# Kernel optimization log

Measured on AMD Instinct MI355X. Metric: run time of the kernel, lower is better.

Reference implementation:

```python
import jax, jax.numpy as jnp
import numpy as np

EPS = 1e-7       # torchvision generalized_box_iou_loss eps
IMG_SIZE = 320.0  # labels are divided by 320 in the original criterion
NO_OBJ = 80       # class id 80 == no-object sentinel


def _hungarian(cost):
    """Jonker-Volgenant style shortest-augmenting-path LSA (== scipy.optimize.linear_sum_assignment).
    cost: [n, m] numpy array, n <= m. Returns (row_ind, col_ind) sorted by row."""
    cost = np.asarray(cost, dtype=np.float64)
    n, m = cost.shape
    INF = float("inf")
    u = np.zeros(n + 1)
    v = np.zeros(m + 1)
    p = np.zeros(m + 1, dtype=np.int64)   # p[j]: 1-based row matched to column j, 0 = free
    way = np.zeros(m + 1, dtype=np.int64)
    for i in range(1, n + 1):
        p[0] = i
        j0 = 0
        minv = np.full(m + 1, INF)
        used = np.zeros(m + 1, dtype=bool)
        while True:
            used[j0] = True
            i0 = p[j0]
            free = ~used[1:]
            cur = cost[i0 - 1] - u[i0] - v[1:]
            better = free & (cur < minv[1:])
            minv[1:] = np.where(better, cur, minv[1:])
            way[1:] = np.where(better, j0, way[1:])
            masked = np.where(free, minv[1:], INF)
            j1 = int(np.argmin(masked)) + 1
            delta = masked[j1 - 1]
            uj = np.nonzero(used)[0]
            u[p[uj]] += delta
            v[uj] -= delta
            minv[1:] = np.where(free, minv[1:] - delta, minv[1:])
            j0 = j1
            if p[j0] == 0:
                break
        while j0 != 0:
            j1 = way[j0]
            p[j0] = p[j1]
            j0 = j1
    cols = np.nonzero(p[1:])[0]
    rows = p[1:][cols] - 1
    order = np.argsort(rows)
    return rows[order], cols[order]


def _box_cxcywh_to_xyxy(b):
    cx, cy, w, h = b[..., 0], b[..., 1], b[..., 2], b[..., 3]
    return jnp.stack([cx - 0.5 * w, cy - 0.5 * h, cx + 0.5 * w, cy + 0.5 * h], axis=-1)


def _cost_matrix(prob_class, predict_bbox, labels):
    """Vectorized version of the original nested double loop: [B, n_pred, n_true] cost."""
    B, P, C = prob_class.shape
    T = labels.shape[1]
    lab_bbox = labels[..., :4] / IMG_SIZE          # [B,T,4] cxcywh in [0,1]
    cls = labels[..., 4].astype(jnp.int32)          # [B,T]

    # class NLL: -log p[b, pred, cls[b, true]]
    logp = jnp.log(prob_class)                      # [B,P,C]
    idx = jnp.broadcast_to(cls[:, None, :], (B, P, T))
    class_nll = -jnp.take_along_axis(logp, idx, axis=2)   # [B,P,T]

    # pairwise L1 (mean over the 4 box coords)
    pb = predict_bbox[:, :, None, :]                # [B,P,1,4]
    lb = lab_bbox[:, None, :, :]                    # [B,1,T,4]
    l1 = jnp.abs(pb - lb).mean(axis=-1)             # [B,P,T]

    # pairwise GIoU loss (1 - GIoU), torchvision convention
    xp = _box_cxcywh_to_xyxy(predict_bbox)[:, :, None, :]   # [B,P,1,4]
    xl = _box_cxcywh_to_xyxy(lab_bbox)[:, None, :, :]       # [B,1,T,4]
    lt = jnp.maximum(xp[..., :2], xl[..., :2])
    rb = jnp.minimum(xp[..., 2:], xl[..., 2:])
    wh = jnp.clip(rb - lt, 0.0)
    inter = wh[..., 0] * wh[..., 1]                          # [B,P,T]
    area_p = (xp[..., 2] - xp[..., 0]) * (xp[..., 3] - xp[..., 1])
    area_l = (xl[..., 2] - xl[..., 0]) * (xl[..., 3] - xl[..., 1])
    union = area_p + area_l - inter
    iou = inter / (union + EPS)
    ltc = jnp.minimum(xp[..., :2], xl[..., :2])
    rbc = jnp.maximum(xp[..., 2:], xl[..., 2:])
    whc = jnp.clip(rbc - ltc, 0.0)
    enclose = whc[..., 0] * whc[..., 1]
    giou = iou - (enclose - union) / (enclose + EPS)
    giou_loss = 1.0 - giou                                   # [B,P,T]

    no_obj_mask = (cls != NO_OBJ).astype(prob_class.dtype)[:, None, :]  # [B,1,T]
    return class_nll + (5.0 * l1 + 2.0 * giou_loss) * no_obj_mask


def setup_inputs() -> dict:
    key = jax.random.key(0)
    k1, k2, k3, k4 = jax.random.split(key, 4)
    B, P, T, C = 64, 150, 150, 81
    prob_class = jax.nn.softmax(jax.random.normal(k1, (B, P, C), jnp.float32), axis=-1)
    predict_bbox = jax.nn.sigmoid(jax.random.normal(k2, (B, P, 4), jnp.float32))
    lab_bbox = jax.random.uniform(k3, (B, T, 4), jnp.float32, 0.05, 0.95) * IMG_SIZE
    lab_cls = jax.random.randint(k4, (B, T), 0, 81).astype(jnp.float32)
    labels = jnp.concatenate([lab_bbox, lab_cls[..., None]], axis=-1)
    return {"prob_class": prob_class, "predict_bbox": predict_bbox, "labels": labels}


def reference(prob_class, predict_bbox, labels):
    cost = _cost_matrix(prob_class, predict_bbox, labels)   # [B,P,T]
    cost_np = np.asarray(cost)
    loss = jnp.zeros((), dtype=cost.dtype)
    for i in range(cost_np.shape[0]):
        r, c = _hungarian(cost_np[i])
        # faithful to the original (it indexes all batch elements with batch-i's matching)
        loss = loss + cost[:, r, c].mean()
    return loss
```

## Files before the change

kernel.cpp:

```cpp
#include <hip/hip_runtime.h>
#include <hip/hip_bf16.h>
#include <math.h>

#define B_   64
#define P_   150
#define T_   150
#define C_   81
#define NOOBJ 80
#define CHAIN_CAP 8
#define ARR_PASSES 3

__global__ void cost_kernel(const float* __restrict__ prob,
                            const float* __restrict__ pbox,
                            const float* __restrict__ labels,
                            float* __restrict__ cost) {
    int idx = blockIdx.x * blockDim.x + threadIdx.x;
    const int total = B_ * P_ * T_;
    if (idx >= total) return;
    int t  = idx % T_;
    int p  = (idx / T_) % P_;
    int b  = idx / (P_ * T_);

    const float* lb5 = labels + ((size_t)b * T_ + t) * 5;
    const float inv = 1.0f / 320.0f;
    float lcx = lb5[0] * inv, lcy = lb5[1] * inv, lw = lb5[2] * inv, lh = lb5[3] * inv;
    int cls = (int)lb5[4];

    const float* pb = pbox + ((size_t)b * P_ + p) * 4;
    float pcx = pb[0], pcy = pb[1], pw = pb[2], ph = pb[3];

    float nll = -logf(prob[((size_t)b * P_ + p) * C_ + cls]);

    float l1 = 0.25f * (fabsf(pcx - lcx) + fabsf(pcy - lcy) +
                        fabsf(pw - lw)   + fabsf(ph - lh));

    float px0 = pcx - 0.5f * pw, py0 = pcy - 0.5f * ph;
    float px1 = pcx + 0.5f * pw, py1 = pcy + 0.5f * ph;
    float lx0 = lcx - 0.5f * lw, ly0 = lcy - 0.5f * lh;
    float lx1 = lcx + 0.5f * lw, ly1 = lcy + 0.5f * lh;

    float ltx = fmaxf(px0, lx0), lty = fmaxf(py0, ly0);
    float rbx = fminf(px1, lx1), rby = fminf(py1, ly1);
    float iw = fmaxf(rbx - ltx, 0.f), ih = fmaxf(rby - lty, 0.f);
    float inter = iw * ih;
    float ap = (px1 - px0) * (py1 - py0);
    float al = (lx1 - lx0) * (ly1 - ly0);
    float un = ap + al - inter;
    float iou = inter / (un + 1e-7f);

    float cx0 = fminf(px0, lx0), cy0 = fminf(py0, ly0);
    float cx1 = fmaxf(px1, lx1), cy1 = fmaxf(py1, ly1);
    float cw = fmaxf(cx1 - cx0, 0.f), ch = fmaxf(cy1 - cy0, 0.f);
    float enc = cw * ch;
    float giou = iou - (enc - un) / (enc + 1e-7f);
    float gl = 1.0f - giou;

    float mask = (cls != NOOBJ) ? 1.0f : 0.0f;
    cost[idx] = nll + (5.0f * l1 + 2.0f * gl) * mask;
}

#define SM_U      (P_ * T_ * 4)
#define SM_TOTAL  (SM_U + 152 * 8)

#define DPPMIN(x, ctrl)                                                          \
    do {                                                                         \
        unsigned _t = (unsigned)__builtin_amdgcn_update_dpp(                     \
            (int)(x), (int)(x), (ctrl), 0xF, 0xF, false);                        \
        (x) = (_t < (x)) ? _t : (x);                                             \
    } while (0)

__device__ __forceinline__ int sel3i(int s, int a, int b, int c) {
    return s == 0 ? a : (s == 1 ? b : c);
}

__device__ __forceinline__ void wave_argmin(double lval, int lpay,
                                            double* oval, int* opay) {
    unsigned key = __float_as_uint((float)lval);
    unsigned x = key;
    DPPMIN(x, 0x111); DPPMIN(x, 0x112); DPPMIN(x, 0x114);
    DPPMIN(x, 0x118); DPPMIN(x, 0x142); DPPMIN(x, 0x143);
    unsigned kmin = (unsigned)__builtin_amdgcn_readlane((int)x, 63);
    unsigned long long cm = __ballot(key == kmin);
    if (__popcll(cm) == 1) {
        int L = (int)__builtin_ctzll(cm);
        int hi = __builtin_amdgcn_readlane(__double2hiint(lval), L);
        int lo = __builtin_amdgcn_readlane(__double2loint(lval), L);
        *oval = __hiloint2double(hi, lo);
        *opay = __builtin_amdgcn_readlane(lpay, L);
    } else {
        double bv = __builtin_inf(); int bp = 0x7FFFFFFF;
        unsigned long long m = cm;
        while (m) {
            int L = (int)__builtin_ctzll(m); m &= m - 1;
            int hi = __builtin_amdgcn_readlane(__double2hiint(lval), L);
            int lo = __builtin_amdgcn_readlane(__double2loint(lval), L);
            double dv = __hiloint2double(hi, lo);
            int dp = __builtin_amdgcn_readlane(lpay, L);
            if (dv < bv || (dv == bv && dp < bp)) { bv = dv; bp = dp; }
        }
        *oval = bv; *opay = bp;
    }
}

__global__ __launch_bounds__(64) void hungarian_kernel(const float* __restrict__ cost,
                                                       int* __restrict__ assign) {
    const int b = blockIdx.x;
    const int lane = threadIdx.x;
    const float* Cg = cost + (size_t)b * (P_ * T_);

    extern __shared__ char smem[];
    float*  cl = (float*)smem;
    double* u  = (double*)(smem + SM_U);

    for (int i4 = lane; i4 < (P_ * T_) / 4; i4 += 64)
        ((float4*)cl)[i4] = ((const float4*)Cg)[i4];
    for (int r = lane; r <= P_; r += 64) u[r] = 0.0;
    __syncthreads();

    const int ja = 1 + lane;
    const int jb = 65 + lane;
    const int jc = 129 + lane;
    const bool va2 = (jc <= T_);
    const int jcs = va2 ? jc : T_;

    const double INF = __builtin_inf();

    float m0 = cl[ja - 1], m1 = cl[jb - 1], m2 = cl[jcs - 1];
    int i1a = 1, i1b = 1, i1c = 1;
    #pragma unroll 4
    for (int r = 2; r <= P_; ++r) {
        int rb_ = (r - 1) * T_;
        float t0 = cl[rb_ + ja - 1], t1 = cl[rb_ + jb - 1], t2 = cl[rb_ + jcs - 1];
        if (t0 < m0) { m0 = t0; i1a = r; }
        if (t1 < m1) { m1 = t1; i1b = r; }
        if (t2 < m2) { m2 = t2; i1c = r; }
    }
    double v0 = (double)m0, v1 = (double)m1, v2 = va2 ? (double)m2 : 0.0;
    int pa = 0, pb = 0, pc = 0;

    int frm = (lane < 22) ? 7 : 3;

    for (int j = 1; j <= T_; ++j) {
        int sl = (j - 1) >> 6, ol = (j - 1) & 63;
        int i1 = __builtin_amdgcn_readlane(sel3i(sl, i1a, i1b, i1c), ol);
        int rl = (i1 - 1) & 63, rs = (i1 - 1) >> 6;
        int fm = __builtin_amdgcn_readlane(frm, rl);
        if (fm & (1 << rs)) {
            if (lane == ol) {
                if (sl == 0) pa = i1; else if (sl == 1) pb = i1; else pc = i1;
            }
            if (lane == rl) frm &= ~(1 << rs);
        }
    }

    for (int pass = 0; pass < ARR_PASSES; ++pass) {
        for (int irow = 1; irow <= P_; ++irow) {
            {
                int rl = (irow - 1) & 63, rs = (irow - 1) >> 6;
                int fm = __builtin_amdgcn_readlane(frm, rl);
                if (!(fm & (1 << rs))) continue;
            }
            int i = irow;
            for (int guard = 0; guard < CHAIN_CAP; ++guard) {
                int base = (i - 1) * T_ - 1;
                float f0 = cl[base + ja], f1 = cl[base + jb], f2 = cl[base + jcs];
                double r0 = (double)f0 - v0;
                double r1 = (double)f1 - v1;
                double r2 = va2 ? ((double)f2 - v2) : INF;
                double lm1, lm2; int lj1, lj2;
                if (r0 <= r1) { lm1 = r0; lj1 = ja; lm2 = r1; lj2 = jb; }
                else          { lm1 = r1; lj1 = jb; lm2 = r0; lj2 = ja; }
                if (r2 < lm1)      { lm2 = lm1; lj2 = lj1; lm1 = r2; lj1 = jc; }
                else if (r2 < lm2) { lm2 = r2; lj2 = jc; }

                double umin; int j1;
                wave_argmin(lm1, lj1, &umin, &j1);
                double s1 = (lj1 == j1) ? lm2 : lm1;
                int    sj = (lj1 == j1) ? lj2 : lj1;
                double usub; int j2;
                wave_argmin(s1, sj, &usub, &j2);

                bool strict = (umin < usub);
                int jt = j1;
                if (strict) {
                    double d = usub - umin;
                    if (lane == ((j1 - 1) & 63)) {
                        int sl = (j1 - 1) >> 6;
                        if (sl == 0) v0 -= d; else if (sl == 1) v1 -= d; else v2 -= d;
                    }
                } else {
                    int sl = (j1 - 1) >> 6, ol = (j1 - 1) & 63;
                    int pj1 = __builtin_amdgcn_readlane(sel3i(sl, pa, pb, pc), ol);
                    if (pj1 != 0) jt = j2;
                }
                int slt = (jt - 1) >> 6, olt = (jt - 1) & 63;
                int k = __builtin_amdgcn_readlane(sel3i(slt, pa, pb, pc), olt);
                if (lane == olt) {
                    if (slt == 0) pa = i; else if (slt == 1) pb = i; else pc = i;
                }
                if (lane == 0) u[i] = strict ? usub : umin;
                { int rl = (i - 1) & 63, rs = (i - 1) >> 6;
                  if (lane == rl) frm &= ~(1 << rs); }
                if (k != 0) {
                    int rl = (k - 1) & 63, rs = (k - 1) >> 6;
                    if (lane == rl) frm |= (1 << rs);
                }
                if (k == 0 || !strict) break;
                i = k;
            }
        }
    }

    for (int i = 1; i <= P_; ++i) {
        {
            int rl = (i - 1) & 63, rs = (i - 1) >> 6;
            int fm = __builtin_amdgcn_readlane(frm, rl);
            if (!(fm & (1 << rs))) continue;
        }
        double mv0 = INF, mv1 = INF, mv2 = INF;
        int w0 = 0, w1 = 0, w2 = 0;
        int um = va2 ? 0 : 4;
        double ua = 0.0, ub = 0.0, uc = 0.0;
        int ra = 0, rb = 0, rc = 0;
        int j0 = 0;
        int i0cur = i;

        double ui0 = u[i];
        double u_i = ui0;
        int base = (i - 1) * T_ - 1;
        float c0 = cl[base + ja];
        float c1 = cl[base + jb];
        float c2 = cl[base + jcs];

        while (true) {
            if (j0 > 0 && lane == ((j0 - 1) & 63)) {
                int sl = (j0 - 1) >> 6;
                if (sl == 0)      { um |= 1; ua = ui0; ra = i0cur; }
                else if (sl == 1) { um |= 2; ub = ui0; rb = i0cur; }
                else              { um |= 4; uc = ui0; rc = i0cur; }
            }

            double cur0 = ((double)c0 - ui0) - v0;
            double cur1 = ((double)c1 - ui0) - v1;
            double cur2 = ((double)c2 - ui0) - v2;
            if (!(um & 1) && cur0 < mv0) { mv0 = cur0; w0 = j0; }
            if (!(um & 2) && cur1 < mv1) { mv1 = cur1; w1 = j0; }
            if (!(um & 4) && cur2 < mv2) { mv2 = cur2; w2 = j0; }

            double bestv = INF; int bestj = 0x7FFFFFFF; int bestp = 0;
            if (!(um & 1))                { bestv = mv0; bestj = ja; bestp = pa; }
            if (!(um & 2) && mv1 < bestv) { bestv = mv1; bestj = jb; bestp = pb; }
            if (!(um & 4) && mv2 < bestv) { bestv = mv2; bestj = jc; bestp = pc; }

            unsigned key = __float_as_uint((float)bestv);
            unsigned x = key;
            DPPMIN(x, 0x111); DPPMIN(x, 0x112); DPPMIN(x, 0x114);
            DPPMIN(x, 0x118); DPPMIN(x, 0x142); DPPMIN(x, 0x143);
            unsigned kmin = (unsigned)__builtin_amdgcn_readlane((int)x, 63);

            unsigned long long cm = __ballot(key == kmin);
            int j1, pj; double delta;
            int pk = (bestp << 8) | (bestj & 0xFF);
            if (__popcll(cm) == 1) {
                int L = (int)__builtin_ctzll(cm);
                int pkw = __builtin_amdgcn_readlane(pk, L);
                j1 = pkw & 0xFF;
                pj = pkw >> 8;
                int hi = __builtin_amdgcn_readlane(__double2hiint(bestv), L);
                int lo = __builtin_amdgcn_readlane(__double2loint(bestv), L);
                delta = __hiloint2double(hi, lo);
            } else {
                double bv = INF; int bj = 0x7FFFFFFF; int bp = 0;
                unsigned long long m = cm;
                while (m) {
                    int L = (int)__builtin_ctzll(m); m &= m - 1;
                    int hi = __builtin_amdgcn_readlane(__double2hiint(bestv), L);
                    int lo = __builtin_amdgcn_readlane(__double2loint(bestv), L);
                    double dv = __hiloint2double(hi, lo);
                    int dj = __builtin_amdgcn_readlane(bestj, L);
                    int dp = __builtin_amdgcn_readlane(bestp, L);
                    if (dv < bv || (dv == bv && dj < bj)) { bv = dv; bj = dj; bp = dp; }
                }
                j1 = bj; pj = bp; delta = bv;
            }

            int pr = (pj > 0) ? pj : 1;
            double ui_n = u[pr];
            int bn = (pr - 1) * T_ - 1;
            float c0n = cl[bn + ja];
            float c1n = cl[bn + jb];
            float c2n = cl[bn + jcs];

            if (um & 1) { v0 -= delta; ua += delta; } else { mv0 -= delta; }
            if (um & 2) { v1 -= delta; ub += delta; } else { mv1 -= delta; }
            if (va2) {
                if (um & 4) { v2 -= delta; uc += delta; } else { mv2 -= delta; }
            }
            u_i += delta;

            i0cur = pj;
            j0 = j1;
            if (pj == 0) break;
            ui0 = ui_n; c0 = c0n; c1 = c1n; c2 = c2n;
        }

        if (um & 1) u[ra] = ua;
        if (um & 2) u[rb] = ub;
        if (va2 && (um & 4)) u[rc] = uc;
        if (lane == 0) u[i] = u_i;

        int jj = j0;
        while (jj != 0) {
            int sj = (jj - 1) >> 6, lj = (jj - 1) & 63;
            int jn = __shfl(sel3i(sj, w0, w1, w2), lj);
            int rown;
            if (jn == 0) rown = i;
            else {
                int sn = (jn - 1) >> 6, ln = (jn - 1) & 63;
                rown = __shfl(sel3i(sn, pa, pb, pc), ln);
            }
            if (lane == lj) {
                if (sj == 0) pa = rown; else if (sj == 1) pb = rown; else pc = rown;
            }
            jj = jn;
        }
    }

    assign[b * P_ + (pa - 1)] = ja - 1;
    assign[b * P_ + (pb - 1)] = jb - 1;
    if (va2) assign[b * P_ + (pc - 1)] = jc - 1;
}

__global__ void gather_kernel(const float* __restrict__ cost,
                              const int* __restrict__ assign,
                              double* __restrict__ partial) {
    const int i = blockIdx.x;
    const int* a = assign + i * P_;
    double s = 0.0;
    for (int idx = threadIdx.x; idx < B_ * P_; idx += blockDim.x) {
        int b = idx / P_;
        int k = idx % P_;
        s += (double)cost[((size_t)b * P_ + k) * T_ + a[k]];
    }
    __shared__ double red[256];
    red[threadIdx.x] = s;
    __syncthreads();
    for (int off = 128; off >= 1; off >>= 1) {
        if (threadIdx.x < off) red[threadIdx.x] += red[threadIdx.x + off];
        __syncthreads();
    }
    if (threadIdx.x == 0) partial[i] = red[0] / (double)(B_ * P_);
}

__global__ void finalize_kernel(const double* __restrict__ partial,
                                float* __restrict__ out) {
    if (threadIdx.x == 0 && blockIdx.x == 0) {
        double s = 0.0;
        for (int i = 0; i < B_; ++i) s += partial[i];
        out[0] = (float)s;
    }
}

extern "C" void kernel_launch(void* const* d_in, const int* in_sizes, int n_in,
                              void* d_out, int out_size, void* d_ws, size_t ws_size,
                              hipStream_t stream) {
    const float* prob   = (const float*)d_in[0];
    const float* pbox   = (const float*)d_in[1];
    const float* labels = (const float*)d_in[2];
    float* out = (float*)d_out;

    char* ws = (char*)d_ws;
    float*  cost    = (float*) ws;
    int*    assign  = (int*)   (ws + (size_t)B_ * P_ * T_ * 4);
    double* partial = (double*)(ws + (size_t)B_ * P_ * T_ * 4 + (size_t)B_ * P_ * 4);

    const int total = B_ * P_ * T_;
    cost_kernel<<<(total + 255) / 256, 256, 0, stream>>>(prob, pbox, labels, cost);

    hungarian_kernel<<<B_, 64, SM_TOTAL, stream>>>(cost, assign);

    gather_kernel<<<B_, 256, 0, stream>>>(cost, assign, partial);

    finalize_kernel<<<1, 64, 0, stream>>>(partial, out);
}
```

Measured before the change: 1.008 ms.

## Store row duals in registers indexed by matched column instead of LDS

Drops the shared-memory u[] array of row potentials and keeps each row's dual in a per-lane register next to the column that row is matched to (qa/qb/qc), plus a free-row dual array (f0/f1/f2). The dual of the next row is now read by cross-lane readlane together with the argmin payload, so the LDS load that used to sit on the serial augmenting-path critical path goes away. The cost is extra readlane and shuffle traffic for doubles, and more register pressure. Duals must also be moved along with assignments during path reversal, which adds bookkeeping that is easy to get wrong.

```diff
diff --git a/kernel.cpp b/kernel.cpp
--- a/kernel.cpp
+++ b/kernel.cpp
@@ -59,8 +59,7 @@
     cost[idx] = nll + (5.0f * l1 + 2.0f * gl) * mask;
 }
 
-#define SM_U      (P_ * T_ * 4)
-#define SM_TOTAL  (SM_U + 152 * 8)
+#define SM_TOTAL  (P_ * T_ * 4)
 
 #define DPPMIN(x, ctrl)                                                          \
     do {                                                                         \
@@ -71,6 +70,19 @@
 
 __device__ __forceinline__ int sel3i(int s, int a, int b, int c) {
     return s == 0 ? a : (s == 1 ? b : c);
+}
+__device__ __forceinline__ double sel3d(int s, double a, double b, double c) {
+    return s == 0 ? a : (s == 1 ? b : c);
+}
+__device__ __forceinline__ double readlane_d(double v, int lane) {
+    int hi = __builtin_amdgcn_readlane(__double2hiint(v), lane);
+    int lo = __builtin_amdgcn_readlane(__double2loint(v), lane);
+    return __hiloint2double(hi, lo);
+}
+__device__ __forceinline__ double shfl_d(double v, int srcLane) {
+    int hi = __shfl(__double2hiint(v), srcLane);
+    int lo = __shfl(__double2loint(v), srcLane);
+    return __hiloint2double(hi, lo);
 }
 
 __device__ __forceinline__ void wave_argmin(double lval, int lpay,
@@ -83,18 +95,14 @@
     unsigned long long cm = __ballot(key == kmin);
     if (__popcll(cm) == 1) {
         int L = (int)__builtin_ctzll(cm);
-        int hi = __builtin_amdgcn_readlane(__double2hiint(lval), L);
-        int lo = __builtin_amdgcn_readlane(__double2loint(lval), L);
-        *oval = __hiloint2double(hi, lo);
+        *oval = readlane_d(lval, L);
         *opay = __builtin_amdgcn_readlane(lpay, L);
     } else {
         double bv = __builtin_inf(); int bp = 0x7FFFFFFF;
         unsigned long long m = cm;
         while (m) {
             int L = (int)__builtin_ctzll(m); m &= m - 1;
-            int hi = __builtin_amdgcn_readlane(__double2hiint(lval), L);
-            int lo = __builtin_amdgcn_readlane(__double2loint(lval), L);
-            double dv = __hiloint2double(hi, lo);
+            double dv = readlane_d(lval, L);
             int dp = __builtin_amdgcn_readlane(lpay, L);
             if (dv < bv || (dv == bv && dp < bp)) { bv = dv; bp = dp; }
         }
@@ -109,12 +117,10 @@
     const float* Cg = cost + (size_t)b * (P_ * T_);
 
     extern __shared__ char smem[];
-    float*  cl = (float*)smem;
-    double* u  = (double*)(smem + SM_U);
+    float* cl = (float*)smem;
 
     for (int i4 = lane; i4 < (P_ * T_) / 4; i4 += 64)
         ((float4*)cl)[i4] = ((const float4*)Cg)[i4];
-    for (int r = lane; r <= P_; r += 64) u[r] = 0.0;
     __syncthreads();
 
     const int ja = 1 + lane;
@@ -137,6 +143,8 @@
     }
     double v0 = (double)m0, v1 = (double)m1, v2 = va2 ? (double)m2 : 0.0;
     int pa = 0, pb = 0, pc = 0;
+    double qa = 0.0, qb = 0.0, qc = 0.0;
+    double f0 = 0.0, f1 = 0.0, f2 = 0.0;
 
     int frm = (lane < 22) ? 7 : 3;
 
@@ -163,10 +171,10 @@
             int i = irow;
             for (int guard = 0; guard < CHAIN_CAP; ++guard) {
                 int base = (i - 1) * T_ - 1;
-                float f0 = cl[base + ja], f1 = cl[base + jb], f2 = cl[base + jcs];
-                double r0 = (double)f0 - v0;
-                double r1 = (double)f1 - v1;
-                double r2 = va2 ? ((double)f2 - v2) : INF;
+                float fc0 = cl[base + ja], fc1 = cl[base + jb], fc2 = cl[base + jcs];
+                double r0 = (double)fc0 - v0;
+                double r1 = (double)fc1 - v1;
+                double r2 = va2 ? ((double)fc2 - v2) : INF;
                 double lm1, lm2; int lj1, lj2;
                 if (r0 <= r1) { lm1 = r0; lj1 = ja; lm2 = r1; lj2 = jb; }
                 else          { lm1 = r1; lj1 = jb; lm2 = r0; lj2 = ja; }
@@ -195,15 +203,23 @@
                 }
                 int slt = (jt - 1) >> 6, olt = (jt - 1) & 63;
                 int k = __builtin_amdgcn_readlane(sel3i(slt, pa, pb, pc), olt);
+                double uk = readlane_d(sel3d(slt, qa, qb, qc), olt);
+                double unew = strict ? usub : umin;
                 if (lane == olt) {
-                    if (slt == 0) pa = i; else if (slt == 1) pb = i; else pc = i;
+                    if (slt == 0) { pa = i; qa = unew; }
+                    else if (slt == 1) { pb = i; qb = unew; }
+                    else { pc = i; qc = unew; }
                 }
-                if (lane == 0) u[i] = strict ? usub : umin;
                 { int rl = (i - 1) & 63, rs = (i - 1) >> 6;
                   if (lane == rl) frm &= ~(1 << rs); }
                 if (k != 0) {
-                    int rl = (k - 1) & 63, rs = (k - 1) >> 6;
-                    if (lane == rl) frm |= (1 << rs);
+                    int kl = (k - 1) & 63, ks = (k - 1) >> 6;
+                    if (lane == kl) {
+                        if (ks == 0)      f0 = uk;
+                        else if (ks == 1) f1 = uk;
+                        else              f2 = uk;
+                        frm |= (1 << ks);
+                    }
                 }
                 if (k == 0 || !strict) break;
                 i = k;
@@ -221,11 +237,13 @@
         int w0 = 0, w1 = 0, w2 = 0;
         int um = va2 ? 0 : 4;
         double ua = 0.0, ub = 0.0, uc = 0.0;
-        int ra = 0, rb = 0, rc = 0;
         int j0 = 0;
-        int i0cur = i;
-
-        double ui0 = u[i];
+
+        double ui0;
+        {
+            int sl = (i - 1) >> 6, ll = (i - 1) & 63;
+            ui0 = readlane_d(sel3d(sl, f0, f1, f2), ll);
+        }
         double u_i = ui0;
         int base = (i - 1) * T_ - 1;
         float c0 = cl[base + ja];
@@ -235,9 +253,9 @@
         while (true) {
             if (j0 > 0 && lane == ((j0 - 1) & 63)) {
                 int sl = (j0 - 1) >> 6;
-                if (sl == 0)      { um |= 1; ua = ui0; ra = i0cur; }
-                else if (sl == 1) { um |= 2; ub = ui0; rb = i0cur; }
-                else              { um |= 4; uc = ui0; rc = i0cur; }
+                if (sl == 0)      { um |= 1; ua = ui0; }
+                else if (sl == 1) { um |= 2; ub = ui0; }
+                else              { um |= 4; uc = ui0; }
             }
 
             double cur0 = ((double)c0 - ui0) - v0;
@@ -248,9 +266,10 @@
             if (!(um & 4) && cur2 < mv2) { mv2 = cur2; w2 = j0; }
 
             double bestv = INF; int bestj = 0x7FFFFFFF; int bestp = 0;
-            if (!(um & 1))                { bestv = mv0; bestj = ja; bestp = pa; }
-            if (!(um & 2) && mv1 < bestv) { bestv = mv1; bestj = jb; bestp = pb; }
-            if (!(um & 4) && mv2 < bestv) { bestv = mv2; bestj = jc; bestp = pc; }
+            double bestq = 0.0;
+            if (!(um & 1))                { bestv = mv0; bestj = ja; bestp = pa; bestq = qa; }
+            if (!(um & 2) && mv1 < bestv) { bestv = mv1; bestj = jb; bestp = pb; bestq = qb; }
+            if (!(um & 4) && mv2 < bestv) { bestv = mv2; bestj = jc; bestp = pc; bestq = qc; }
 
             unsigned key = __float_as_uint((float)bestv);
             unsigned x = key;
@@ -259,33 +278,30 @@
             unsigned kmin = (unsigned)__builtin_amdgcn_readlane((int)x, 63);
 
             unsigned long long cm = __ballot(key == kmin);
-            int j1, pj; double delta;
+            int j1, pj; double delta, upj;
             int pk = (bestp << 8) | (bestj & 0xFF);
             if (__popcll(cm) == 1) {
                 int L = (int)__builtin_ctzll(cm);
                 int pkw = __builtin_amdgcn_readlane(pk, L);
                 j1 = pkw & 0xFF;
                 pj = pkw >> 8;
-                int hi = __builtin_amdgcn_readlane(__double2hiint(bestv), L);
-                int lo = __builtin_amdgcn_readlane(__double2loint(bestv), L);
-                delta = __hiloint2double(hi, lo);
+                delta = readlane_d(bestv, L);
+                upj   = readlane_d(bestq, L);
             } else {
-                double bv = INF; int bj = 0x7FFFFFFF; int bp = 0;
+                double bv = INF; int bj = 0x7FFFFFFF; int bp = 0; double bq = 0.0;
                 unsigned long long m = cm;
                 while (m) {
                     int L = (int)__builtin_ctzll(m); m &= m - 1;
-                    int hi = __builtin_amdgcn_readlane(__double2hiint(bestv), L);
-                    int lo = __builtin_amdgcn_readlane(__double2loint(bestv), L);
-                    double dv = __hiloint2double(hi, lo);
+                    double dv = readlane_d(bestv, L);
                     int dj = __builtin_amdgcn_readlane(bestj, L);
                     int dp = __builtin_amdgcn_readlane(bestp, L);
-                    if (dv < bv || (dv == bv && dj < bj)) { bv = dv; bj = dj; bp = dp; }
+                    double dq = readlane_d(bestq, L);
+                    if (dv < bv || (dv == bv && dj < bj)) { bv = dv; bj = dj; bp = dp; bq = dq; }
                 }
-                j1 = bj; pj = bp; delta = bv;
+                j1 = bj; pj = bp; delta = bv; upj = bq;
             }
 
             int pr = (pj > 0) ? pj : 1;
-            double ui_n = u[pr];
             int bn = (pr - 1) * T_ - 1;
             float c0n = cl[bn + ja];
             float c1n = cl[bn + jb];
@@ -298,29 +314,30 @@
             }
             u_i += delta;
 
-            i0cur = pj;
             j0 = j1;
             if (pj == 0) break;
-            ui0 = ui_n; c0 = c0n; c1 = c1n; c2 = c2n;
-        }
-
-        if (um & 1) u[ra] = ua;
-        if (um & 2) u[rb] = ub;
-        if (va2 && (um & 4)) u[rc] = uc;
-        if (lane == 0) u[i] = u_i;
+            ui0 = upj; c0 = c0n; c1 = c1n; c2 = c2n;
+        }
+
+        if (um & 1) qa = ua;
+        if (um & 2) qb = ub;
+        if (va2 && (um & 4)) qc = uc;
 
         int jj = j0;
         while (jj != 0) {
             int sj = (jj - 1) >> 6, lj = (jj - 1) & 63;
             int jn = __shfl(sel3i(sj, w0, w1, w2), lj);
-            int rown;
-            if (jn == 0) rown = i;
+            int rown; double rowu;
+            if (jn == 0) { rown = i; rowu = u_i; }
             else {
                 int sn = (jn - 1) >> 6, ln = (jn - 1) & 63;
                 rown = __shfl(sel3i(sn, pa, pb, pc), ln);
+                rowu = shfl_d(sel3d(sn, ua, ub, uc), ln);
             }
             if (lane == lj) {
-                if (sj == 0) pa = rown; else if (sj == 1) pb = rown; else pc = rown;
+                if (sj == 0)      { pa = rown; qa = rowu; }
+                else if (sj == 1) { pb = rown; qb = rowu; }
+                else              { pc = rown; qc = rowu; }
             }
             jj = jn;
         }
```

Result: slower. 1.063 ms (+5.5%).
